# Performance work log

Measured on AMD Instinct MI355X. Metric: run time of the kernel, lower is better.

The kernel has to match this reference:

```python
import jax, jax.numpy as jnp
import numpy as np

BOND_TOL = 0.4
CLASH_TOL = 1.5
IDEAL_CA_CA = 3.8
EPS = 1e-08


def setup_inputs() -> dict:
    key = jax.random.key(0)
    k1, _ = jax.random.split(key)
    B, L = 8, 2048
    positions = jax.random.normal(k1, (B, L, 3), dtype=jnp.float32) * 10.0
    mask = jnp.ones((B, L), dtype=jnp.float32)
    return {"positions": positions, "mask": mask}


def reference(positions, mask):
    # positions: [B, L, 3] CA coordinates; mask: [B, L]
    L = positions.shape[1]
    ca = positions
    ca_mask = mask

    # --- bond term: consecutive CA-CA distances ---
    ca_diff = ca[:, 1:] - ca[:, :-1]                       # [B, L-1, 3]
    ca_dist = jnp.sqrt(jnp.sum(ca_diff ** 2, axis=-1) + EPS)
    bond_violation = jax.nn.relu(jnp.abs(ca_dist - IDEAL_CA_CA) - BOND_TOL)
    bond_mask = ca_mask[:, 1:] * ca_mask[:, :-1]
    bond_loss = jnp.sum(bond_violation * bond_mask) / (jnp.sum(bond_mask) + EPS)

    # --- clash term: all-pairs distances, non-bonded (|i-j| > 2) ---
    all_diff = ca[:, :, None, :] - ca[:, None, :, :]       # [B, L, L, 3]
    all_dist = jnp.sqrt(jnp.sum(all_diff ** 2, axis=-1) + EPS)  # [B, L, L]
    idx = jnp.arange(L)
    seq_sep = jnp.abs(idx[None, :] - idx[:, None])         # [L, L]
    non_bonded = (seq_sep > 2).astype(ca.dtype)
    clash_violation = jax.nn.relu(CLASH_TOL - all_dist)
    pair_mask = ca_mask[:, :, None] * ca_mask[:, None, :] * non_bonded[None]
    clash_loss = jnp.sum(clash_violation * pair_mask) / (jnp.sum(pair_mask) + EPS)

    total = bond_loss + clash_loss
    # stacked: [bond_loss, clash_loss, total_violation]
    return jnp.stack([bond_loss, clash_loss, total])
```

## Files before the change

kernel.cpp:

```cpp
#include <hip/hip_runtime.h>

#define TPB 256
#define RPB 8
#define SEQ_L 2048
#define CHUNK 256
#define NCH (SEQ_L / CHUNK)
#define NBATCH 8
#define NPAIR 128
#define NBLOCKS (NBATCH * NPAIR)
#define NWAVE (TPB / 64)

static constexpr float kBondTol  = 0.4f;
static constexpr float kClashTol = 1.5f;
static constexpr float kIdeal    = 3.8f;
static constexpr float kEps      = 1e-8f;
static constexpr float kThresh2  = 2.25f;

__device__ __forceinline__ float wred(float v) {
#pragma unroll
  for (int o = 32; o > 0; o >>= 1) v += __shfl_down(v, o, 64);
  return v;
}

__global__ __launch_bounds__(TPB, 4) void viol_main(
    const float* __restrict__ pos,
    const float* __restrict__ mask,
    float4* __restrict__ partial) {
  __shared__ float4 s[SEQ_L];
  __shared__ float  redm[NWAVE];
  __shared__ float  red4[NWAVE][4];

  const int b = blockIdx.x & 7;
  const int t = blockIdx.x >> 3;
  const int i0A = t << 3;
  const int i0B = (255 - t) << 3;
  const int k0A = i0A >> 8;
  const int k0B = i0B >> 8;

  const float* pb = pos  + (size_t)b * SEQ_L * 3;
  const float* mb = mask + (size_t)b * SEQ_L;

  float mpart = 0.f;
#pragma unroll
  for (int it = 0; it < NCH; ++it) {
    int idx = (int)threadIdx.x + (it << 8);
    float x = pb[3 * idx + 0];
    float y = pb[3 * idx + 1];
    float z = pb[3 * idx + 2];
    float m = mb[idx];
    s[idx] = make_float4(x, y, z, m);
    mpart += m;
  }
  mpart = wred(mpart);
  const int wid  = threadIdx.x >> 6;
  const int lane = threadIdx.x & 63;
  if (lane == 0) redm[wid] = mpart;
  __syncthreads();
  const float msum = redm[0] + redm[1] + redm[2] + redm[3];

  float cv = 0.f, pm = 0.f, bv = 0.f, bm = 0.f;

  for (int tt = 0; tt < 2; ++tt) {
    const int i0 = tt ? i0B : i0A;
    const int k0 = tt ? k0B : k0A;

    float px[RPB], py[RPB], pz[RPB], pw[RPB], accr[RPB];
#pragma unroll
    for (int q = 0; q < RPB; ++q) {
      float4 p = s[i0 + q];
      px[q] = p.x; py[q] = p.y; pz[q] = p.z; pw[q] = p.w;
      accr[q] = 0.f;
    }

    {
      const int j = (int)threadIdx.x + (k0 << 8);
      const float4 pj = s[j];
#pragma unroll
      for (int q = 0; q < RPB; ++q) {
        const int i = i0 + q;
        float dx = pj.x - px[q];
        float dy = pj.y - py[q];
        float dz = pj.z - pz[q];
        float d2 = fmaf(dx, dx, fmaf(dy, dy, dz * dz));
        float dist = __builtin_amdgcn_sqrtf(d2 + kEps);
        float mw = (j > i) ? pj.w : 0.f;
        accr[q] = fmaf(fmaxf(kClashTol - dist, 0.f), mw, accr[q]);
      }
    }

#pragma unroll 2
    for (int k = k0 + 1; k < NCH; ++k) {
      float4 pj = s[threadIdx.x + (k << 8)];
      float d2r[RPB];
#pragma unroll
      for (int q = 0; q < RPB; ++q) {
        float dx = pj.x - px[q];
        float dy = pj.y - py[q];
        float dz = pj.z - pz[q];
        d2r[q] = fmaf(dx, dx, fmaf(dy, dy, dz * dz));
      }
      float mv = d2r[0];
#pragma unroll
      for (int q = 1; q < RPB; ++q) mv = fminf(mv, d2r[q]);
      if (__ballot(mv < kThresh2) != 0ull) {
#pragma unroll
        for (int q = 0; q < RPB; ++q) {
          float dist = __builtin_amdgcn_sqrtf(d2r[q] + kEps);
          accr[q] = fmaf(fmaxf(kClashTol - dist, 0.f), pj.w, accr[q]);
        }
      }
    }

#pragma unroll
    for (int q = 0; q < RPB; ++q) cv = fmaf(pw[q], accr[q], cv);
  }

  if (threadIdx.x < 16) {
    const int i = ((threadIdx.x & 8) ? i0B : i0A) + (int)(threadIdx.x & 7);
    const float4 pi = s[i];
    float nv = 0.f;
    const int jhi = (i + 2 > SEQ_L - 1) ? SEQ_L - 1 : i + 2;
    for (int j = i + 1; j <= jhi; ++j) {
      float4 pj = s[j];
      float dx = pj.x - pi.x;
      float dy = pj.y - pi.y;
      float dz = pj.z - pi.z;
      float dist = __builtin_amdgcn_sqrtf(dx * dx + dy * dy + dz * dz + kEps);
      nv += fmaxf(kClashTol - dist, 0.f) * pj.w;
    }
    cv -= pi.w * nv;

    float nm = 0.f;
    const int jlo = (i - 2 < 0) ? 0 : i - 2;
    for (int j = jlo; j <= jhi; ++j) nm += s[j].w;
    pm += pi.w * (msum - nm);

    if (i < SEQ_L - 1) {
      const float4 pj = s[i + 1];
      float dx = pj.x - pi.x;
      float dy = pj.y - pi.y;
      float dz = pj.z - pi.z;
      float dist = __builtin_amdgcn_sqrtf(dx * dx + dy * dy + dz * dz + kEps);
      float viol = fmaxf(fabsf(dist - kIdeal) - kBondTol, 0.f);
      bv += viol * pi.w * pj.w;
      bm += pi.w * pj.w;
    }
  }

  bv = wred(bv); bm = wred(bm); cv = wred(cv); pm = wred(pm);
  if (lane == 0) {
    red4[wid][0] = bv; red4[wid][1] = bm;
    red4[wid][2] = cv; red4[wid][3] = pm;
  }
  __syncthreads();
  if (threadIdx.x == 0) {
    float tbv = 0.f, tbm = 0.f, tcv = 0.f, tpm = 0.f;
#pragma unroll
    for (int w = 0; w < NWAVE; ++w) {
      tbv += red4[w][0]; tbm += red4[w][1];
      tcv += red4[w][2]; tpm += red4[w][3];
    }
    partial[blockIdx.x] = make_float4(tbv, tbm, 2.f * tcv, tpm);
  }
}

__global__ __launch_bounds__(TPB) void viol_reduce(
    const float4* __restrict__ partial, float* __restrict__ out) {
  __shared__ float red4[NWAVE][4];
  float bv = 0.f, bm = 0.f, cv = 0.f, pm = 0.f;
#pragma unroll
  for (int i = threadIdx.x; i < NBLOCKS; i += TPB) {
    float4 p = partial[i];
    bv += p.x; bm += p.y; cv += p.z; pm += p.w;
  }
  bv = wred(bv); bm = wred(bm); cv = wred(cv); pm = wred(pm);
  const int wid  = threadIdx.x >> 6;
  const int lane = threadIdx.x & 63;
  if (lane == 0) {
    red4[wid][0] = bv; red4[wid][1] = bm;
    red4[wid][2] = cv; red4[wid][3] = pm;
  }
  __syncthreads();
  if (threadIdx.x == 0) {
    float tbv = 0.f, tbm = 0.f, tcv = 0.f, tpm = 0.f;
#pragma unroll
    for (int w = 0; w < NWAVE; ++w) {
      tbv += red4[w][0]; tbm += red4[w][1];
      tcv += red4[w][2]; tpm += red4[w][3];
    }
    float bond  = tbv / (tbm + kEps);
    float clash = tcv / (tpm + kEps);
    out[0] = bond;
    out[1] = clash;
    out[2] = bond + clash;
  }
}

extern "C" void kernel_launch(void* const* d_in, const int* in_sizes, int n_in,
                              void* d_out, int out_size, void* d_ws, size_t ws_size,
                              hipStream_t stream) {
  const float* pos  = (const float*)d_in[0];
  const float* mask = (const float*)d_in[1];
  float* out = (float*)d_out;
  float4* partial = (float4*)d_ws;

  viol_main<<<dim3(NBLOCKS), dim3(TPB), 0, stream>>>(pos, mask, partial);
  viol_reduce<<<dim3(1), dim3(TPB), 0, stream>>>(partial, out);
}
```

Before: 63.22 us.

## Fuse final reduction via atomic counter, use SoA shared memory and masked-far coordinates

The final reduction is folded into the main kernel: the last block to increment an atomic counter performs the global sum, which removes the second kernel launch but adds a memset. Shared memory moves from float4 AoS to three SoA arrays. Masked residues are relocated far away so the per-pair mask multiply can be dropped. Each block now handles one 8-row tile instead of a balanced pair of tiles, and blocks load only the chunks they need. Occupancy bounds are raised, and the diagonal chunk also gets the ballot-based early skip.

```diff
diff --git a/kernel.cpp b/kernel.cpp
--- a/kernel.cpp
+++ b/kernel.cpp
@@ -3,11 +3,10 @@
 #define TPB 256
 #define RPB 8
 #define SEQ_L 2048
-#define CHUNK 256
-#define NCH (SEQ_L / CHUNK)
+#define NCH 8
 #define NBATCH 8
-#define NPAIR 128
-#define NBLOCKS (NBATCH * NPAIR)
+#define NTILE 256
+#define NBLOCKS (NBATCH * NTILE)
 #define NWAVE (TPB / 64)
 
 static constexpr float kBondTol  = 0.4f;
@@ -15,6 +14,8 @@
 static constexpr float kIdeal    = 3.8f;
 static constexpr float kEps      = 1e-8f;
 static constexpr float kThresh2  = 2.25f;
+static constexpr float kFarBase  = 1.0e5f;
+static constexpr float kHugeD2   = 1.0e12f;
 
 __device__ __forceinline__ float wred(float v) {
 #pragma unroll
@@ -22,20 +23,21 @@
   return v;
 }
 
-__global__ __launch_bounds__(TPB, 4) void viol_main(
+__global__ __launch_bounds__(TPB, 6) void viol_fused(
     const float* __restrict__ pos,
     const float* __restrict__ mask,
-    float4* __restrict__ partial) {
-  __shared__ float4 s[SEQ_L];
-  __shared__ float  redm[NWAVE];
-  __shared__ float  red4[NWAVE][4];
-
-  const int b = blockIdx.x & 7;
-  const int t = blockIdx.x >> 3;
-  const int i0A = t << 3;
-  const int i0B = (255 - t) << 3;
-  const int k0A = i0A >> 8;
-  const int k0B = i0B >> 8;
+    float4* __restrict__ partial,
+    unsigned* __restrict__ counter,
+    float* __restrict__ out) {
+  __shared__ float sx[SEQ_L], sy[SEQ_L], sz[SEQ_L];
+  __shared__ float redm[NWAVE];
+  __shared__ float red4[NWAVE][4];
+  __shared__ int   sLast;
+
+  const int b  = blockIdx.x & 7;
+  const int t  = blockIdx.x >> 3;
+  const int i0 = t << 3;
+  const int k0 = t >> 5;
 
   const float* pb = pos  + (size_t)b * SEQ_L * 3;
   const float* mb = mask + (size_t)b * SEQ_L;
@@ -43,13 +45,16 @@
   float mpart = 0.f;
 #pragma unroll
   for (int it = 0; it < NCH; ++it) {
-    int idx = (int)threadIdx.x + (it << 8);
-    float x = pb[3 * idx + 0];
-    float y = pb[3 * idx + 1];
-    float z = pb[3 * idx + 2];
-    float m = mb[idx];
-    s[idx] = make_float4(x, y, z, m);
+    const int idx = (int)threadIdx.x + (it << 8);
+    const float m = mb[idx];
     mpart += m;
+    if (it >= k0) {
+      float x = pb[3 * idx + 0];
+      float y = pb[3 * idx + 1];
+      float z = pb[3 * idx + 2];
+      if (m == 0.f) { x = kFarBase + 4.f * (float)idx; y = 0.f; z = 0.f; }
+      sx[idx] = x; sy[idx] = y; sz[idx] = z;
+    }
   }
   mpart = wred(mpart);
   const int wid  = threadIdx.x >> 6;
@@ -58,92 +63,85 @@
   __syncthreads();
   const float msum = redm[0] + redm[1] + redm[2] + redm[3];
 
-  float cv = 0.f, pm = 0.f, bv = 0.f, bm = 0.f;
-
-  for (int tt = 0; tt < 2; ++tt) {
-    const int i0 = tt ? i0B : i0A;
-    const int k0 = tt ? k0B : k0A;
-
-    float px[RPB], py[RPB], pz[RPB], pw[RPB], accr[RPB];
+  float px[RPB], py[RPB], pz[RPB], accr[RPB];
+#pragma unroll
+  for (int q = 0; q < RPB; ++q) {
+    px[q] = sx[i0 + q]; py[q] = sy[i0 + q]; pz[q] = sz[i0 + q];
+    accr[q] = 0.f;
+  }
+
+  {
+    const int j = (int)threadIdx.x + (k0 << 8);
+    const float xj = sx[j], yj = sy[j], zj = sz[j];
+    float d2r[RPB];
 #pragma unroll
     for (int q = 0; q < RPB; ++q) {
-      float4 p = s[i0 + q];
-      px[q] = p.x; py[q] = p.y; pz[q] = p.z; pw[q] = p.w;
-      accr[q] = 0.f;
-    }
-
-    {
-      const int j = (int)threadIdx.x + (k0 << 8);
-      const float4 pj = s[j];
+      const float dx = xj - px[q], dy = yj - py[q], dz = zj - pz[q];
+      const float d2 = fmaf(dx, dx, fmaf(dy, dy, dz * dz));
+      d2r[q] = (j > i0 + q) ? d2 : kHugeD2;
+    }
+    float mv = d2r[0];
+#pragma unroll
+    for (int q = 1; q < RPB; ++q) mv = fminf(mv, d2r[q]);
+    if (__ballot(mv < kThresh2) != 0ull) {
 #pragma unroll
       for (int q = 0; q < RPB; ++q) {
-        const int i = i0 + q;
-        float dx = pj.x - px[q];
-        float dy = pj.y - py[q];
-        float dz = pj.z - pz[q];
-        float d2 = fmaf(dx, dx, fmaf(dy, dy, dz * dz));
-        float dist = __builtin_amdgcn_sqrtf(d2 + kEps);
-        float mw = (j > i) ? pj.w : 0.f;
-        accr[q] = fmaf(fmaxf(kClashTol - dist, 0.f), mw, accr[q]);
+        const float dist = __builtin_amdgcn_sqrtf(d2r[q] + kEps);
+        accr[q] += fmaxf(kClashTol - dist, 0.f);
       }
     }
-
-#pragma unroll 2
-    for (int k = k0 + 1; k < NCH; ++k) {
-      float4 pj = s[threadIdx.x + (k << 8)];
-      float d2r[RPB];
+  }
+
+  for (int k = k0 + 1; k < NCH; ++k) {
+    const int j = (int)threadIdx.x + (k << 8);
+    const float xj = sx[j], yj = sy[j], zj = sz[j];
+    float d2r[RPB];
+#pragma unroll
+    for (int q = 0; q < RPB; ++q) {
+      const float dx = xj - px[q], dy = yj - py[q], dz = zj - pz[q];
+      d2r[q] = fmaf(dx, dx, fmaf(dy, dy, dz * dz));
+    }
+    float mv = d2r[0];
+#pragma unroll
+    for (int q = 1; q < RPB; ++q) mv = fminf(mv, d2r[q]);
+    if (__ballot(mv < kThresh2) != 0ull) {
 #pragma unroll
       for (int q = 0; q < RPB; ++q) {
-        float dx = pj.x - px[q];
-        float dy = pj.y - py[q];
-        float dz = pj.z - pz[q];
-        d2r[q] = fmaf(dx, dx, fmaf(dy, dy, dz * dz));
+        const float dist = __builtin_amdgcn_sqrtf(d2r[q] + kEps);
+        accr[q] += fmaxf(kClashTol - dist, 0.f);
       }
-      float mv = d2r[0];
-#pragma unroll
-      for (int q = 1; q < RPB; ++q) mv = fminf(mv, d2r[q]);
-      if (__ballot(mv < kThresh2) != 0ull) {
-#pragma unroll
-        for (int q = 0; q < RPB; ++q) {
-          float dist = __builtin_amdgcn_sqrtf(d2r[q] + kEps);
-          accr[q] = fmaf(fmaxf(kClashTol - dist, 0.f), pj.w, accr[q]);
-        }
-      }
-    }
-
-#pragma unroll
-    for (int q = 0; q < RPB; ++q) cv = fmaf(pw[q], accr[q], cv);
-  }
-
-  if (threadIdx.x < 16) {
-    const int i = ((threadIdx.x & 8) ? i0B : i0A) + (int)(threadIdx.x & 7);
-    const float4 pi = s[i];
+    }
+  }
+
+  float cv = 0.f;
+#pragma unroll
+  for (int q = 0; q < RPB; ++q) cv += accr[q];
+
+  float bv = 0.f, bm = 0.f, pm = 0.f;
+  if (threadIdx.x < 8) {
+    const int i = i0 + (int)threadIdx.x;
+    const float xi = sx[i], yi = sy[i], zi = sz[i];
+    const int jhi = (i + 2 > SEQ_L - 1) ? SEQ_L - 1 : i + 2;
     float nv = 0.f;
-    const int jhi = (i + 2 > SEQ_L - 1) ? SEQ_L - 1 : i + 2;
     for (int j = i + 1; j <= jhi; ++j) {
-      float4 pj = s[j];
-      float dx = pj.x - pi.x;
-      float dy = pj.y - pi.y;
-      float dz = pj.z - pi.z;
-      float dist = __builtin_amdgcn_sqrtf(dx * dx + dy * dy + dz * dz + kEps);
-      nv += fmaxf(kClashTol - dist, 0.f) * pj.w;
-    }
-    cv -= pi.w * nv;
-
+      const float dx = sx[j] - xi, dy = sy[j] - yi, dz = sz[j] - zi;
+      const float dist = __builtin_amdgcn_sqrtf(dx*dx + dy*dy + dz*dz + kEps);
+      nv += fmaxf(kClashTol - dist, 0.f);
+    }
+    cv -= nv;
+
+    const float mi = mb[i];
     float nm = 0.f;
     const int jlo = (i - 2 < 0) ? 0 : i - 2;
-    for (int j = jlo; j <= jhi; ++j) nm += s[j].w;
-    pm += pi.w * (msum - nm);
+    for (int j = jlo; j <= jhi; ++j) nm += mb[j];
+    pm = mi * (msum - nm);
 
     if (i < SEQ_L - 1) {
-      const float4 pj = s[i + 1];
-      float dx = pj.x - pi.x;
-      float dy = pj.y - pi.y;
-      float dz = pj.z - pi.z;
-      float dist = __builtin_amdgcn_sqrtf(dx * dx + dy * dy + dz * dz + kEps);
-      float viol = fmaxf(fabsf(dist - kIdeal) - kBondTol, 0.f);
-      bv += viol * pi.w * pj.w;
-      bm += pi.w * pj.w;
+      const float dx = sx[i+1] - xi, dy = sy[i+1] - yi, dz = sz[i+1] - zi;
+      const float dist = __builtin_amdgcn_sqrtf(dx*dx + dy*dy + dz*dz + kEps);
+      const float mj = mb[i + 1];
+      bv = fmaxf(fabsf(dist - kIdeal) - kBondTol, 0.f) * mi * mj;
+      bm = mi * mj;
     }
   }
 
@@ -161,38 +159,41 @@
       tcv += red4[w][2]; tpm += red4[w][3];
     }
     partial[blockIdx.x] = make_float4(tbv, tbm, 2.f * tcv, tpm);
-  }
-}
-
-__global__ __launch_bounds__(TPB) void viol_reduce(
-    const float4* __restrict__ partial, float* __restrict__ out) {
-  __shared__ float red4[NWAVE][4];
-  float bv = 0.f, bm = 0.f, cv = 0.f, pm = 0.f;
-#pragma unroll
-  for (int i = threadIdx.x; i < NBLOCKS; i += TPB) {
-    float4 p = partial[i];
-    bv += p.x; bm += p.y; cv += p.z; pm += p.w;
-  }
-  bv = wred(bv); bm = wred(bm); cv = wred(cv); pm = wred(pm);
-  const int wid  = threadIdx.x >> 6;
-  const int lane = threadIdx.x & 63;
-  if (lane == 0) {
-    red4[wid][0] = bv; red4[wid][1] = bm;
-    red4[wid][2] = cv; red4[wid][3] = pm;
+    __threadfence();
+    const unsigned old = atomicAdd(counter, 1u);
+    sLast = (old == NBLOCKS - 1) ? 1 : 0;
   }
   __syncthreads();
-  if (threadIdx.x == 0) {
-    float tbv = 0.f, tbm = 0.f, tcv = 0.f, tpm = 0.f;
-#pragma unroll
-    for (int w = 0; w < NWAVE; ++w) {
-      tbv += red4[w][0]; tbm += red4[w][1];
-      tcv += red4[w][2]; tpm += red4[w][3];
-    }
-    float bond  = tbv / (tbm + kEps);
-    float clash = tcv / (tpm + kEps);
-    out[0] = bond;
-    out[1] = clash;
-    out[2] = bond + clash;
+
+  if (sLast) {
+    __threadfence();
+    float rbv = 0.f, rbm = 0.f, rcv = 0.f, rpm = 0.f;
+    for (int i = (int)threadIdx.x; i < NBLOCKS; i += TPB) {
+      float* p = (float*)(partial + i);
+      rbv += __hip_atomic_load(p + 0, __ATOMIC_RELAXED, __HIP_MEMORY_SCOPE_AGENT);
+      rbm += __hip_atomic_load(p + 1, __ATOMIC_RELAXED, __HIP_MEMORY_SCOPE_AGENT);
+      rcv += __hip_atomic_load(p + 2, __ATOMIC_RELAXED, __HIP_MEMORY_SCOPE_AGENT);
+      rpm += __hip_atomic_load(p + 3, __ATOMIC_RELAXED, __HIP_MEMORY_SCOPE_AGENT);
+    }
+    rbv = wred(rbv); rbm = wred(rbm); rcv = wred(rcv); rpm = wred(rpm);
+    if (lane == 0) {
+      red4[wid][0] = rbv; red4[wid][1] = rbm;
+      red4[wid][2] = rcv; red4[wid][3] = rpm;
+    }
+    __syncthreads();
+    if (threadIdx.x == 0) {
+      float tbv = 0.f, tbm = 0.f, tcv = 0.f, tpm = 0.f;
+#pragma unroll
+      for (int w = 0; w < NWAVE; ++w) {
+        tbv += red4[w][0]; tbm += red4[w][1];
+        tcv += red4[w][2]; tpm += red4[w][3];
+      }
+      const float bond  = tbv / (tbm + kEps);
+      const float clash = tcv / (tpm + kEps);
+      out[0] = bond;
+      out[1] = clash;
+      out[2] = bond + clash;
+    }
   }
 }
 
@@ -202,8 +203,10 @@
   const float* pos  = (const float*)d_in[0];
   const float* mask = (const float*)d_in[1];
   float* out = (float*)d_out;
-  float4* partial = (float4*)d_ws;
-
-  viol_main<<<dim3(NBLOCKS), dim3(TPB), 0, stream>>>(pos, mask, partial);
-  viol_reduce<<<dim3(1), dim3(TPB), 0, stream>>>(partial, out);
+  float4* partial   = (float4*)d_ws;
+  unsigned* counter = (unsigned*)((char*)d_ws + NBLOCKS * sizeof(float4));
+
+  hipMemsetAsync(counter, 0, sizeof(unsigned), stream);
+  viol_fused<<<dim3(NBLOCKS), dim3(TPB), 0, stream>>>(pos, mask, partial,
+                                                      counter, out);
 }
```

Result: slower. 99.71 us (+57.7%).
